# Optimization experiments

Hardware: AMD Instinct MI355X
Metric: run time of the kernel (lower is better)

## Reference

```python
import jax, jax.numpy as jnp
import numpy as np

D = 64   # input_dim = number of tiny MLPs
H = 64   # hidden_dim
L = 2    # num_hidden_layers
B = 32768


def setup_inputs() -> dict:
    key = jax.random.key(0)
    ks = jax.random.split(key, 14)
    s = 0.1
    return {
        "x": jax.random.normal(ks[0], (B, 2 * D), dtype=jnp.float32),
        # bank of D tiny MLPs, params stacked along leading expert dim
        "h_w1": jax.random.normal(ks[1], (D, H), dtype=jnp.float32) * s,   # Linear(1,H) weight per expert
        "h_b1": jax.random.normal(ks[2], (D, H), dtype=jnp.float32) * s,
        "h_wh": jax.random.normal(ks[3], (L, D, H, H), dtype=jnp.float32) * s,
        "h_bh": jax.random.normal(ks[4], (L, D, H), dtype=jnp.float32) * s,
        "h_wo": jax.random.normal(ks[5], (D, H), dtype=jnp.float32) * s,   # Linear(H,1) weight per expert
        "h_bo": jax.random.normal(ks[6], (D,), dtype=jnp.float32) * s,
        # larger model_g MLP
        "g_w1": jax.random.normal(ks[7], (D, H), dtype=jnp.float32) * s,
        "g_b1": jax.random.normal(ks[8], (H,), dtype=jnp.float32) * s,
        "g_wh": jax.random.normal(ks[9], (L, H, H), dtype=jnp.float32) * s,
        "g_bh": jax.random.normal(ks[10], (L, H), dtype=jnp.float32) * s,
        "g_wo": jax.random.normal(ks[11], (H,), dtype=jnp.float32) * s,
        "g_bo": jax.random.normal(ks[12], (1,), dtype=jnp.float32) * s,
    }


def reference(x, h_w1, h_b1, h_wh, h_bh, h_wo, h_bo,
              g_w1, g_b1, g_wh, g_bh, g_wo, g_bo):
    first = x[:, :D]    # [B, D] -> model_g input
    second = x[:, D:]   # [B, D] -> one scalar column per tiny MLP

    # --- bank of D tiny MLPs, fused as batched GEMMs over expert dim d ---
    # input layer: Linear(1,H): h[b,d,:] = relu(second[b,d] * w1[d,:] + b1[d,:])
    h = jax.nn.relu(second[:, :, None] * h_w1[None, :, :] + h_b1[None, :, :])  # [B,D,H]
    for l in range(L):
        h = jax.nn.relu(jnp.einsum('bdh,dhk->bdk', h, h_wh[l]) + h_bh[l][None, :, :])
    h_out = jnp.einsum('bdh,dh->bd', h, h_wo) + h_bo[None, :]  # [B, D]

    # --- model_g: standard MLP on first half ---
    g = jax.nn.relu(first @ g_w1 + g_b1)          # [B, H]
    for l in range(L):
        g = jax.nn.relu(g @ g_wh[l] + g_bh[l])
    g_out = g @ g_wo[:, None] + g_bo              # [B, 1]

    return h_out, g_out
```

## Files before the change

### kernel.cpp

```cpp
#include <hip/hip_runtime.h>

typedef __attribute__((ext_vector_type(4))) float  f32x4;
typedef __attribute__((ext_vector_type(8))) __bf16 bf16x8;
typedef __attribute__((ext_vector_type(4))) __bf16 bf16x4;

#define LDA 72

__global__ void reformat_w(const float* __restrict__ h_wh,
                           const float* __restrict__ g_w1,
                           const float* __restrict__ g_wh,
                           __bf16* __restrict__ wsH,
                           __bf16* __restrict__ wsG)
{
  int i = blockIdx.x * 256 + threadIdx.x;
  int j = i & 7, lane = (i >> 3) & 63, f = (i >> 9) & 7;
  int c = lane & 15, g4 = lane >> 4, mf = f >> 1, kk = f & 1;
  int krow = (kk << 5) + (g4 << 3) + j;
  int mcol = (mf << 4) + c;
  if (i < 524288) {
    int ld = i >> 12;
    wsH[i] = (__bf16)h_wh[(ld << 12) + (krow << 6) + mcol];
  } else if (i < 524288 + 12288) {
    int t = i - 524288;
    int lg = t >> 12;
    const float* W = (lg == 0) ? g_w1 : g_wh + ((lg - 1) << 12);
    wsG[t] = (__bf16)W[(krow << 6) + mcol];
  }
}

__global__ __launch_bounds__(256, 4) void fused_nn(
    const float* __restrict__ x,
    const float* __restrict__ h_w1, const float* __restrict__ h_b1,
    const float* __restrict__ h_bh,
    const float* __restrict__ h_wo, const float* __restrict__ h_bo,
    const float* __restrict__ g_b1,
    const float* __restrict__ g_bh,
    const float* __restrict__ g_wo, const float* __restrict__ g_bo,
    const __bf16* __restrict__ wsH, const __bf16* __restrict__ wsG,
    float* __restrict__ out, int nTiles, int Btot)
{
  __shared__ __align__(16) __bf16 sA[256 * LDA];
  __shared__ __align__(16) float  sLB[3][64];
  __shared__ __align__(16) float  sWo[64];
  __shared__ __align__(16) float  sV1[64];
  __shared__ __align__(16) float  sV2[64];
  __shared__ float  sS[256];

  const int tid  = threadIdx.x;
  const int lane = tid & 63;
  const int wid  = tid >> 6;
  const int c    = lane & 15;
  const int g4   = lane >> 4;
  const int wn   = wid << 6;

  const int bid  = blockIdx.x;
  const bool is_h = (bid < (nTiles << 6));
  int d = 0, tile;
  if (is_h) { d = bid / nTiles; tile = bid - d * nTiles; }
  else      { tile = bid - (nTiles << 6); }
  const int row0 = tile << 8;
  const int nMM  = is_h ? 2 : 3;

  if (is_h) {
    if (tid < 64) {
      sLB[0][tid] = h_bh[(d << 6) + tid];
      sLB[1][tid] = h_bh[((64 + d) << 6) + tid];
      sWo[tid]    = h_wo[(d << 6) + tid];
      sV1[tid]    = h_w1[(d << 6) + tid];
      sV2[tid]    = h_b1[(d << 6) + tid];
    }
    sS[tid] = x[(row0 + tid) * 128 + 64 + d];
    __syncthreads();
    const int c0 = (tid & 7) << 3;
    const f32x4 w1a = *(const f32x4*)&sV1[c0];
    const f32x4 w1b = *(const f32x4*)&sV1[c0 + 4];
    const f32x4 b1a = *(const f32x4*)&sV2[c0];
    const f32x4 b1b = *(const f32x4*)&sV2[c0 + 4];
    #pragma unroll
    for (int i = 0; i < 8; ++i) {
      int row = (i << 5) + (tid >> 3);
      float s = sS[row];
      bf16x8 v;
      #pragma unroll
      for (int j = 0; j < 4; ++j) {
        v[j]     = (__bf16)fmaxf(fmaf(s, w1a[j], b1a[j]), 0.f);
        v[j + 4] = (__bf16)fmaxf(fmaf(s, w1b[j], b1b[j]), 0.f);
      }
      *(bf16x8*)&sA[row * LDA + c0] = v;
    }
  } else {
    if (tid < 64) {
      sLB[0][tid] = g_b1[tid];
      sLB[1][tid] = g_bh[tid];
      sLB[2][tid] = g_bh[64 + tid];
      sWo[tid]    = g_wo[tid];
    }
    #pragma unroll
    for (int i = 0; i < 16; ++i) {
      int u = (i << 8) + tid;
      int row = u >> 4, c4 = (u & 15) << 2;
      const float4 v = *(const float4*)&x[(row0 + row) * 128 + c4];
      bf16x4 b;
      b[0] = (__bf16)v.x; b[1] = (__bf16)v.y; b[2] = (__bf16)v.z; b[3] = (__bf16)v.w;
      *(bf16x4*)&sA[row * LDA + c4] = b;
    }
  }
  __syncthreads();

  f32x4 acc[4][4];
  for (int l = 0; l < nMM; ++l) {
    const __bf16* wfrag = is_h ? (wsH + (((l << 6) + d) << 12)) : (wsG + (l << 12));

    #pragma unroll
    for (int mf = 0; mf < 4; ++mf) {
      f32x4 bv = *(const f32x4*)&sLB[l][(mf << 4) + (g4 << 2)];
      #pragma unroll
      for (int nf = 0; nf < 4; ++nf) acc[mf][nf] = bv;
    }

    #pragma unroll
    for (int kk = 0; kk < 2; ++kk) {
      bf16x8 aw[4], bh[4];
      #pragma unroll
      for (int mf = 0; mf < 4; ++mf)
        aw[mf] = *(const bf16x8*)&wfrag[((((mf << 1) | kk)) << 9) + (lane << 3)];
      #pragma unroll
      for (int nf = 0; nf < 4; ++nf)
        bh[nf] = *(const bf16x8*)&sA[(wn + (nf << 4) + c) * LDA + (kk << 5) + (g4 << 3)];
      #pragma unroll
      for (int mf = 0; mf < 4; ++mf)
        #pragma unroll
        for (int nf = 0; nf < 4; ++nf)
          acc[mf][nf] = __builtin_amdgcn_mfma_f32_16x16x32_bf16(aw[mf], bh[nf], acc[mf][nf], 0, 0, 0);
    }

    if (l < nMM - 1) {
      __syncthreads();
      #pragma unroll
      for (int mf = 0; mf < 4; ++mf)
        #pragma unroll
        for (int nf = 0; nf < 4; ++nf) {
          bf16x4 v;
          #pragma unroll
          for (int r = 0; r < 4; ++r) v[r] = (__bf16)fmaxf(acc[mf][nf][r], 0.f);
          *(bf16x4*)&sA[(wn + (nf << 4) + c) * LDA + (mf << 4) + (g4 << 2)] = v;
        }
      __syncthreads();
    }
  }

  float p[4] = {0.f, 0.f, 0.f, 0.f};
  #pragma unroll
  for (int mf = 0; mf < 4; ++mf) {
    f32x4 wv = *(const f32x4*)&sWo[(mf << 4) + (g4 << 2)];
    #pragma unroll
    for (int nf = 0; nf < 4; ++nf)
      #pragma unroll
      for (int r = 0; r < 4; ++r)
        p[nf] += fmaxf(acc[mf][nf][r], 0.f) * wv[r];
  }
  #pragma unroll
  for (int nf = 0; nf < 4; ++nf) {
    p[nf] += __shfl_xor(p[nf], 16);
    p[nf] += __shfl_xor(p[nf], 32);
  }
  float sel = (g4 == 0) ? p[0] : (g4 == 1) ? p[1] : (g4 == 2) ? p[2] : p[3];
  int batch = row0 + wn + lane;
  float ob  = is_h ? h_bo[d] : g_bo[0];
  if (is_h) out[(batch << 6) + d]   = sel + ob;
  else      out[(Btot << 6) + batch] = sel + ob;
}

extern "C" void kernel_launch(void* const* d_in, const int* in_sizes, int n_in,
                              void* d_out, int out_size, void* d_ws, size_t ws_size,
                              hipStream_t stream) {
  const float* x    = (const float*)d_in[0];
  const float* h_w1 = (const float*)d_in[1];
  const float* h_b1 = (const float*)d_in[2];
  const float* h_wh = (const float*)d_in[3];
  const float* h_bh = (const float*)d_in[4];
  const float* h_wo = (const float*)d_in[5];
  const float* h_bo = (const float*)d_in[6];
  const float* g_w1 = (const float*)d_in[7];
  const float* g_b1 = (const float*)d_in[8];
  const float* g_wh = (const float*)d_in[9];
  const float* g_bh = (const float*)d_in[10];
  const float* g_wo = (const float*)d_in[11];
  const float* g_bo = (const float*)d_in[12];

  __bf16* wsH = (__bf16*)d_ws;
  __bf16* wsG = (__bf16*)((char*)d_ws + 2 * 64 * 4096 * 2);

  const int Btot   = in_sizes[0] / 128;
  const int nTiles = Btot >> 8;

  hipLaunchKernelGGL(reformat_w, dim3(2096), dim3(256), 0, stream,
                     h_wh, g_w1, g_wh, wsH, wsG);

  dim3 grid(nTiles * 65), block(256);
  hipLaunchKernelGGL(fused_nn, grid, block, 0, stream,
                     x, h_w1, h_b1, h_bh, h_wo, h_bo,
                     g_b1, g_bh, g_wo, g_bo,
                     (const __bf16*)wsH, (const __bf16*)wsG,
                     (float*)d_out, nTiles, Btot);
}
```

Measured before the change: 67.15 us.

## Keep inter-layer activations in registers via permuted weight columns, drop LDS

The hidden-dimension columns of the pre-formatted weights are permuted so that an MFMA output fragment maps directly onto the B-operand fragment of the next layer. Activations can then stay in registers between layers, which removes the shared-memory round trips and the __syncthreads barriers. The first layer is built straight from global x loads into register fragments. The block order is also interleaved so the 64 tiny-MLP blocks and the g block for the same batch tile are adjacent. The cost is higher register pressure and uncoalesced strided x loads for the h branch.

Measured after the change: 96.15 us. 43.2% more time.

```diff
diff --git a/kernel.cpp b/kernel.cpp
--- a/kernel.cpp
+++ b/kernel.cpp
@@ -2,9 +2,10 @@
 
 typedef __attribute__((ext_vector_type(4))) float  f32x4;
 typedef __attribute__((ext_vector_type(8))) __bf16 bf16x8;
-typedef __attribute__((ext_vector_type(4))) __bf16 bf16x4;
-
-#define LDA 72
+
+__device__ __forceinline__ int Pq(int q) {
+  return ((q >> 5) << 5) + (((q >> 2) & 3) << 3) + (((q >> 4) & 1) << 2) + (q & 3);
+}
 
 __global__ void reformat_w(const float* __restrict__ h_wh,
                            const float* __restrict__ g_w1,
@@ -16,15 +17,54 @@
   int j = i & 7, lane = (i >> 3) & 63, f = (i >> 9) & 7;
   int c = lane & 15, g4 = lane >> 4, mf = f >> 1, kk = f & 1;
   int krow = (kk << 5) + (g4 << 3) + j;
-  int mcol = (mf << 4) + c;
+  int mcol = Pq((mf << 4) + c);
   if (i < 524288) {
     int ld = i >> 12;
     wsH[i] = (__bf16)h_wh[(ld << 12) + (krow << 6) + mcol];
-  } else if (i < 524288 + 12288) {
+  } else if (i < 536576) {
     int t = i - 524288;
     int lg = t >> 12;
     const float* W = (lg == 0) ? g_w1 : g_wh + ((lg - 1) << 12);
     wsG[t] = (__bf16)W[(krow << 6) + mcol];
+  }
+}
+
+__device__ __forceinline__ void layer(const __bf16* __restrict__ wf,
+                                      const float* __restrict__ bias,
+                                      int lane, int g4, bool rebuild,
+                                      f32x4 (&acc)[4][4], bf16x8 (&bfr)[4][2])
+{
+  bf16x8 aw0[4], aw1[4];
+  #pragma unroll
+  for (int mf = 0; mf < 4; ++mf) {
+    aw0[mf] = *(const bf16x8*)&wf[((mf << 1) << 9) + (lane << 3)];
+    aw1[mf] = *(const bf16x8*)&wf[(((mf << 1) | 1) << 9) + (lane << 3)];
+  }
+  f32x4 bv[4];
+  #pragma unroll
+  for (int mf = 0; mf < 4; ++mf)
+    bv[mf] = *(const f32x4*)&bias[((mf >> 1) << 5) + (g4 << 3) + ((mf & 1) << 2)];
+  #pragma unroll
+  for (int mf = 0; mf < 4; ++mf)
+    #pragma unroll
+    for (int nf = 0; nf < 4; ++nf)
+      acc[mf][nf] = __builtin_amdgcn_mfma_f32_16x16x32_bf16(aw0[mf], bfr[nf][0], bv[mf], 0, 0, 0);
+  #pragma unroll
+  for (int mf = 0; mf < 4; ++mf)
+    #pragma unroll
+    for (int nf = 0; nf < 4; ++nf)
+      acc[mf][nf] = __builtin_amdgcn_mfma_f32_16x16x32_bf16(aw1[mf], bfr[nf][1], acc[mf][nf], 0, 0, 0);
+  if (rebuild) {
+    #pragma unroll
+    for (int nf = 0; nf < 4; ++nf)
+      #pragma unroll
+      for (int kk = 0; kk < 2; ++kk) {
+        bf16x8 v;
+        #pragma unroll
+        for (int e = 0; e < 8; ++e)
+          v[e] = (__bf16)fmaxf(acc[(kk << 1) | (e >> 2)][nf][e & 3], 0.f);
+        bfr[nf][kk] = v;
+      }
   }
 }
 
@@ -33,142 +73,97 @@
     const float* __restrict__ h_w1, const float* __restrict__ h_b1,
     const float* __restrict__ h_bh,
     const float* __restrict__ h_wo, const float* __restrict__ h_bo,
-    const float* __restrict__ g_b1,
-    const float* __restrict__ g_bh,
+    const float* __restrict__ g_b1, const float* __restrict__ g_bh,
     const float* __restrict__ g_wo, const float* __restrict__ g_bo,
     const __bf16* __restrict__ wsH, const __bf16* __restrict__ wsG,
-    float* __restrict__ out, int nTiles, int Btot)
+    float* __restrict__ out, int Btot)
 {
-  __shared__ __align__(16) __bf16 sA[256 * LDA];
-  __shared__ __align__(16) float  sLB[3][64];
-  __shared__ __align__(16) float  sWo[64];
-  __shared__ __align__(16) float  sV1[64];
-  __shared__ __align__(16) float  sV2[64];
-  __shared__ float  sS[256];
-
   const int tid  = threadIdx.x;
   const int lane = tid & 63;
   const int wid  = tid >> 6;
   const int c    = lane & 15;
   const int g4   = lane >> 4;
-  const int wn   = wid << 6;
 
   const int bid  = blockIdx.x;
-  const bool is_h = (bid < (nTiles << 6));
-  int d = 0, tile;
-  if (is_h) { d = bid / nTiles; tile = bid - d * nTiles; }
-  else      { tile = bid - (nTiles << 6); }
-  const int row0 = tile << 8;
-  const int nMM  = is_h ? 2 : 3;
+  const int tile = bid / 65;
+  const int sub  = bid - tile * 65;
+  const bool is_h = (sub < 64);
+  const int d    = sub & 63;
+  const int nb   = (tile << 8) + (wid << 6);
+
+  f32x4  acc[4][4];
+  bf16x8 bfr[4][2];
 
   if (is_h) {
-    if (tid < 64) {
-      sLB[0][tid] = h_bh[(d << 6) + tid];
-      sLB[1][tid] = h_bh[((64 + d) << 6) + tid];
-      sWo[tid]    = h_wo[(d << 6) + tid];
-      sV1[tid]    = h_w1[(d << 6) + tid];
-      sV2[tid]    = h_b1[(d << 6) + tid];
+    const float* w1p = h_w1 + (d << 6);
+    const float* b1p = h_b1 + (d << 6);
+    f32x4 w1v[2][2], b1v[2][2];
+    #pragma unroll
+    for (int kk = 0; kk < 2; ++kk)
+      #pragma unroll
+      for (int h = 0; h < 2; ++h) {
+        int off = (kk << 5) + (g4 << 3) + (h << 2);
+        w1v[kk][h] = *(const f32x4*)&w1p[off];
+        b1v[kk][h] = *(const f32x4*)&b1p[off];
+      }
+    #pragma unroll
+    for (int nf = 0; nf < 4; ++nf) {
+      float s = x[(size_t)(nb + (nf << 4) + c) * 128 + 64 + d];
+      #pragma unroll
+      for (int kk = 0; kk < 2; ++kk) {
+        bf16x8 v;
+        #pragma unroll
+        for (int h = 0; h < 2; ++h)
+          #pragma unroll
+          for (int r = 0; r < 4; ++r)
+            v[(h << 2) + r] = (__bf16)fmaxf(fmaf(s, w1v[kk][h][r], b1v[kk][h][r]), 0.f);
+        bfr[nf][kk] = v;
+      }
     }
-    sS[tid] = x[(row0 + tid) * 128 + 64 + d];
-    __syncthreads();
-    const int c0 = (tid & 7) << 3;
-    const f32x4 w1a = *(const f32x4*)&sV1[c0];
-    const f32x4 w1b = *(const f32x4*)&sV1[c0 + 4];
-    const f32x4 b1a = *(const f32x4*)&sV2[c0];
-    const f32x4 b1b = *(const f32x4*)&sV2[c0 + 4];
-    #pragma unroll
-    for (int i = 0; i < 8; ++i) {
-      int row = (i << 5) + (tid >> 3);
-      float s = sS[row];
-      bf16x8 v;
-      #pragma unroll
-      for (int j = 0; j < 4; ++j) {
-        v[j]     = (__bf16)fmaxf(fmaf(s, w1a[j], b1a[j]), 0.f);
-        v[j + 4] = (__bf16)fmaxf(fmaf(s, w1b[j], b1b[j]), 0.f);
-      }
-      *(bf16x8*)&sA[row * LDA + c0] = v;
+    layer(wsH + (d << 12),        h_bh + (d << 6),        lane, g4, true,  acc, bfr);
+    layer(wsH + ((64 + d) << 12), h_bh + ((64 + d) << 6), lane, g4, false, acc, bfr);
+  } else {
+    #pragma unroll
+    for (int nf = 0; nf < 4; ++nf) {
+      const float* xr = x + (size_t)(nb + (nf << 4) + c) * 128;
+      #pragma unroll
+      for (int kk = 0; kk < 2; ++kk) {
+        f32x4 v0 = *(const f32x4*)&xr[(kk << 5) + (g4 << 3)];
+        f32x4 v1 = *(const f32x4*)&xr[(kk << 5) + (g4 << 3) + 4];
+        bf16x8 v;
+        #pragma unroll
+        for (int r = 0; r < 4; ++r) { v[r] = (__bf16)v0[r]; v[4 + r] = (__bf16)v1[r]; }
+        bfr[nf][kk] = v;
+      }
     }
-  } else {
-    if (tid < 64) {
-      sLB[0][tid] = g_b1[tid];
-      sLB[1][tid] = g_bh[tid];
-      sLB[2][tid] = g_bh[64 + tid];
-      sWo[tid]    = g_wo[tid];
-    }
-    #pragma unroll
-    for (int i = 0; i < 16; ++i) {
-      int u = (i << 8) + tid;
-      int row = u >> 4, c4 = (u & 15) << 2;
-      const float4 v = *(const float4*)&x[(row0 + row) * 128 + c4];
-      bf16x4 b;
-      b[0] = (__bf16)v.x; b[1] = (__bf16)v.y; b[2] = (__bf16)v.z; b[3] = (__bf16)v.w;
-      *(bf16x4*)&sA[row * LDA + c4] = b;
-    }
-  }
-  __syncthreads();
-
-  f32x4 acc[4][4];
-  for (int l = 0; l < nMM; ++l) {
-    const __bf16* wfrag = is_h ? (wsH + (((l << 6) + d) << 12)) : (wsG + (l << 12));
-
-    #pragma unroll
-    for (int mf = 0; mf < 4; ++mf) {
-      f32x4 bv = *(const f32x4*)&sLB[l][(mf << 4) + (g4 << 2)];
-      #pragma unroll
-      for (int nf = 0; nf < 4; ++nf) acc[mf][nf] = bv;
-    }
-
-    #pragma unroll
-    for (int kk = 0; kk < 2; ++kk) {
-      bf16x8 aw[4], bh[4];
-      #pragma unroll
-      for (int mf = 0; mf < 4; ++mf)
-        aw[mf] = *(const bf16x8*)&wfrag[((((mf << 1) | kk)) << 9) + (lane << 3)];
-      #pragma unroll
-      for (int nf = 0; nf < 4; ++nf)
-        bh[nf] = *(const bf16x8*)&sA[(wn + (nf << 4) + c) * LDA + (kk << 5) + (g4 << 3)];
-      #pragma unroll
-      for (int mf = 0; mf < 4; ++mf)
-        #pragma unroll
-        for (int nf = 0; nf < 4; ++nf)
-          acc[mf][nf] = __builtin_amdgcn_mfma_f32_16x16x32_bf16(aw[mf], bh[nf], acc[mf][nf], 0, 0, 0);
-    }
-
-    if (l < nMM - 1) {
-      __syncthreads();
-      #pragma unroll
-      for (int mf = 0; mf < 4; ++mf)
-        #pragma unroll
-        for (int nf = 0; nf < 4; ++nf) {
-          bf16x4 v;
-          #pragma unroll
-          for (int r = 0; r < 4; ++r) v[r] = (__bf16)fmaxf(acc[mf][nf][r], 0.f);
-          *(bf16x4*)&sA[(wn + (nf << 4) + c) * LDA + (mf << 4) + (g4 << 2)] = v;
-        }
-      __syncthreads();
-    }
-  }
-
+    layer(wsG,        g_b1,      lane, g4, true,  acc, bfr);
+    layer(wsG + 4096, g_bh,      lane, g4, true,  acc, bfr);
+    layer(wsG + 8192, g_bh + 64, lane, g4, false, acc, bfr);
+  }
+
+  const float* wo = is_h ? h_wo + (d << 6) : g_wo;
+  const float  ob = is_h ? h_bo[d] : g_bo[0];
+  f32x4 wv[4];
+  #pragma unroll
+  for (int mf = 0; mf < 4; ++mf)
+    wv[mf] = *(const f32x4*)&wo[((mf >> 1) << 5) + (g4 << 3) + ((mf & 1) << 2)];
   float p[4] = {0.f, 0.f, 0.f, 0.f};
   #pragma unroll
-  for (int mf = 0; mf < 4; ++mf) {
-    f32x4 wv = *(const f32x4*)&sWo[(mf << 4) + (g4 << 2)];
+  for (int mf = 0; mf < 4; ++mf)
     #pragma unroll
     for (int nf = 0; nf < 4; ++nf)
       #pragma unroll
       for (int r = 0; r < 4; ++r)
-        p[nf] += fmaxf(acc[mf][nf][r], 0.f) * wv[r];
-  }
+        p[nf] += fmaxf(acc[mf][nf][r], 0.f) * wv[mf][r];
   #pragma unroll
   for (int nf = 0; nf < 4; ++nf) {
     p[nf] += __shfl_xor(p[nf], 16);
     p[nf] += __shfl_xor(p[nf], 32);
   }
   float sel = (g4 == 0) ? p[0] : (g4 == 1) ? p[1] : (g4 == 2) ? p[2] : p[3];
-  int batch = row0 + wn + lane;
-  float ob  = is_h ? h_bo[d] : g_bo[0];
-  if (is_h) out[(batch << 6) + d]   = sel + ob;
-  else      out[(Btot << 6) + batch] = sel + ob;
+  int batch = nb + lane;
+  if (is_h) out[((size_t)batch << 6) + d]   = sel + ob;
+  else      out[((size_t)Btot << 6) + batch] = sel + ob;
 }
 
 extern "C" void kernel_launch(void* const* d_in, const int* in_sizes, int n_in,
@@ -197,10 +192,9 @@
   hipLaunchKernelGGL(reformat_w, dim3(2096), dim3(256), 0, stream,
                      h_wh, g_w1, g_wh, wsH, wsG);
 
-  dim3 grid(nTiles * 65), block(256);
-  hipLaunchKernelGGL(fused_nn, grid, block, 0, stream,
+  hipLaunchKernelGGL(fused_nn, dim3(nTiles * 65), dim3(256), 0, stream,
                      x, h_w1, h_b1, h_bh, h_wo, h_bo,
                      g_b1, g_bh, g_wo, g_bo,
                      (const __bf16*)wsH, (const __bf16*)wsG,
-                     (float*)d_out, nTiles, Btot);
-}
+                     (float*)d_out, Btot);
+}
```
